# Kernel optimization log

Hardware: AMD Instinct MI355X
Metric: run time of the kernel (lower is better)

Reference implementation:

```python
import jax, jax.numpy as jnp
import numpy as np

LATENT = 256


def setup_inputs() -> dict:
    key = jax.random.key(0)
    ks = jax.random.split(key, 10)
    B, T, V, E, D0, H, L = 512, 200, 3356, 1128, 20000, 1024, LATENT

    def glorot(k, shape):
        fan_out, fan_in = shape
        std = np.sqrt(2.0 / (fan_in + fan_out)).astype(np.float32)
        return jax.random.normal(k, shape, dtype=jnp.float32) * std

    x = jax.random.uniform(ks[0], (B, D0), dtype=jnp.float32)
    item_ids = jax.random.randint(ks[1], (B, T), 0, V, dtype=jnp.int32)
    embed = jax.random.normal(ks[2], (V, E), dtype=jnp.float32)
    Wi = glorot(ks[3], (L, E))
    bi = jnp.zeros((L,), jnp.float32)
    We1 = glorot(ks[4], (H, D0))
    be1 = jnp.zeros((H,), jnp.float32)
    We2 = glorot(ks[5], (2 * L, H))
    be2 = jnp.zeros((2 * L,), jnp.float32)
    Wd1 = glorot(ks[6], (H, L))
    bd1 = jnp.zeros((H,), jnp.float32)
    Wd2 = glorot(ks[7], (D0, H))
    bd2 = jnp.zeros((D0,), jnp.float32)
    # dropout(p=0.5) mask, pre-scaled by 1/(1-p)=2
    drop_mask = (jax.random.bernoulli(ks[8], 0.5, (B, D0))).astype(jnp.float32) * 2.0
    eps = jax.random.normal(ks[9], (B, L), dtype=jnp.float32)
    return {"x": x, "item_ids": item_ids, "embed": embed, "Wi": Wi, "bi": bi,
            "We1": We1, "be1": be1, "We2": We2, "be2": be2,
            "Wd1": Wd1, "bd1": bd1, "Wd2": Wd2, "bd2": bd2,
            "drop_mask": drop_mask, "eps": eps}


def reference(x, item_ids, embed, Wi, bi, We1, be1, We2, be2,
              Wd1, bd1, Wd2, bd2, drop_mask, eps):
    # item feature path: embedding lookup -> linear -> per-sequence stats
    item = jnp.einsum('bte,le->btl', embed[item_ids], Wi) + bi        # [B,T,L]
    mean = jnp.mean(item, axis=1)                                      # [B,L]
    deviation = jnp.std(item, axis=1, ddof=1)                          # torch.std (unbiased)

    # encoder: F.normalize (L2 over features) -> dropout -> tanh MLP
    xn = x / jnp.maximum(jnp.linalg.norm(x, axis=1, keepdims=True), 1e-12)
    h = xn * drop_mask
    h = jnp.tanh(h @ We1.T + be1)
    gparams = h @ We2.T + be2                                          # [B,2L]
    mu, logvar = gparams[:, :LATENT], gparams[:, LATENT:]

    # reparam: MVN with diagonal covariance diag(deviation) == mean + sqrt(dev)*eps
    prior = mean + jnp.sqrt(deviation) * eps
    z = prior * jnp.exp(0.5 * logvar) + mu

    # decoder: tanh MLP
    hd = jnp.tanh(z @ Wd1.T + bd1)
    recon_x = hd @ Wd2.T + bd2                                         # [B,D0]
    return recon_x, mu, logvar
```

## Files before the change

kernel.cpp:

```cpp
#include <hip/hip_runtime.h>
#include <hip/hip_bf16.h>

typedef __bf16 bf16x8 __attribute__((ext_vector_type(8)));
typedef float f32x4 __attribute__((ext_vector_type(4)));
typedef unsigned short u16x8 __attribute__((ext_vector_type(8)));
typedef unsigned int u32x4 __attribute__((ext_vector_type(4)));

static __device__ __forceinline__ unsigned short f2bf(float f){
  unsigned int u = __float_as_uint(f);
  u += 0x7fffu + ((u >> 16) & 1u);
  return (unsigned short)(u >> 16);
}

static __device__ __forceinline__ unsigned int cvtpk(float lo, float hi){
  unsigned int r;
  asm("v_cvt_pk_bf16_f32 %0, %1, %2" : "=v"(r) : "v"(lo), "v"(hi));
  return r;
}

static __device__ __forceinline__ u16x8 cvt8(const float4& a, const float4& b){
  u16x8 r;
  r[0]=f2bf(a.x); r[1]=f2bf(a.y); r[2]=f2bf(a.z); r[3]=f2bf(a.w);
  r[4]=f2bf(b.x); r[5]=f2bf(b.y); r[6]=f2bf(b.z); r[7]=f2bf(b.w);
  return r;
}

static __device__ __forceinline__ void gload16(const void* g, void* l){
  __builtin_amdgcn_global_load_lds(
      (const __attribute__((address_space(1))) unsigned int*)g,
      (__attribute__((address_space(3))) unsigned int*)l, 16, 0, 0);
}

template<int EPI>
__global__ __launch_bounds__(256, 2) void gemm_bigf(
    const unsigned short* __restrict__ A, const float* __restrict__ Bw,
    const float* __restrict__ bias,
    float* __restrict__ Cf, unsigned short* __restrict__ Cbf,
    int M, int N, int K, int kchunk)
{
  constexpr int BK = 32, BUFB = 8192 + 16384;
  __shared__ char smem[3 * BUFB];

  const int tid  = threadIdx.x, lane = tid & 63, wave = tid >> 6;
  const int bm0  = blockIdx.y * 128, bn0 = blockIdx.x * 128;
  const int k0   = blockIdx.z * kchunk;
  const int kend = min(K, k0 + kchunk);
  const int nk   = (kend - k0) / BK;
  const int fr = lane & 15, fq = lane >> 4;
  const int wm = (wave >> 1) * 64, wn = (wave & 1) * 64;

  const int ar_off = wave * 16 + (lane >> 2), ac_off = (lane & 3) * 8;
  const int br_off = wave * 8 + (lane >> 3);
  const int bg_off = (((lane & 7) ^ (lane >> 3)) << 2);

  auto stage = [&](int buf, int t){
    char* base = smem + buf * BUFB;
    const int kk = k0 + t * BK;
    #pragma unroll
    for (int c = 0; c < 2; c++) {
      const int r = min(bm0 + c * 64 + ar_off, M - 1);
      gload16(A + (size_t)r * K + kk + ac_off, base + c * 4096 + wave * 1024);
    }
    #pragma unroll
    for (int c = 0; c < 4; c++) {
      const int r = min(bn0 + c * 32 + br_off, N - 1);
      gload16(Bw + (size_t)r * K + kk + bg_off, base + 8192 + c * 4096 + wave * 1024);
    }
  };

  stage(0, 0);
  if (nk > 1) stage(1, 1);
  if (nk > 2) stage(2, 2);

  f32x4 acc[4][4] = {};
  int cur = 0;

  for (int t = 0; t < nk; ++t) {
    const int rem = nk - t - 1;
    if (rem >= 2)      asm volatile("s_waitcnt vmcnt(12)" ::: "memory");
    else if (rem == 1) asm volatile("s_waitcnt vmcnt(6)"  ::: "memory");
    else               asm volatile("s_waitcnt vmcnt(0)"  ::: "memory");
    __builtin_amdgcn_s_barrier();
    __builtin_amdgcn_sched_barrier(0);

    const unsigned short* lA = (const unsigned short*)(smem + cur * BUFB);
    const char*           lB = smem + cur * BUFB + 8192;
    u16x8 af[4], bg[4];
    #pragma unroll
    for (int i = 0; i < 4; i++) af[i] = *(const u16x8*)&lA[(wm + i*16 + fr) * BK + fq * 8];
    #pragma unroll
    for (int j = 0; j < 4; j++) {
      const int r  = wn + j*16 + fr;
      const int s0 = (((fq << 1) ^ (r & 7)) << 4);
      const char* bp = lB + r * 128;
      f32x4 u = *(const f32x4*)(bp + s0);
      f32x4 v = *(const f32x4*)(bp + (s0 ^ 16));
      u32x4 wv; wv[0]=cvtpk(u[0],u[1]); wv[1]=cvtpk(u[2],u[3]);
                wv[2]=cvtpk(v[0],v[1]); wv[3]=cvtpk(v[2],v[3]);
      bg[j] = __builtin_bit_cast(u16x8, wv);
    }
    asm volatile("s_waitcnt lgkmcnt(0)" ::: "memory");
    __builtin_amdgcn_sched_barrier(0);
    __builtin_amdgcn_s_barrier();
    if (t + 3 < nk) stage(cur, t + 3);

    #pragma unroll
    for (int i = 0; i < 4; i++)
      #pragma unroll
      for (int j = 0; j < 4; j++)
        acc[i][j] = __builtin_amdgcn_mfma_f32_16x16x32_bf16(
            __builtin_bit_cast(bf16x8, af[i]),
            __builtin_bit_cast(bf16x8, bg[j]),
            acc[i][j], 0, 0, 0);
    cur = (cur == 2) ? 0 : cur + 1;
  }

  #pragma unroll
  for (int i = 0; i < 4; i++)
    #pragma unroll
    for (int j = 0; j < 4; j++)
      #pragma unroll
      for (int r = 0; r < 4; r++) {
        int row = bm0 + wm + i*16 + fq*4 + r;
        int col = bn0 + wn + j*16 + fr;
        if (row < M && col < N) {
          float v = acc[i][j][r];
          if constexpr (EPI == 0) {
            Cf[(size_t)row * N + col] = v + (bias ? bias[col] : 0.0f);
          } else if constexpr (EPI == 1) {
            atomicAdd(&Cf[(size_t)row * N + col], v);
          } else {
            Cbf[(size_t)row * N + col] = f2bf(tanhf(v + bias[col]));
          }
        }
      }
}

template<int EPI>
__global__ __launch_bounds__(256) void gemm_sm(
    const unsigned short* __restrict__ A, const unsigned short* __restrict__ Bw,
    const float* __restrict__ bias,
    float* __restrict__ Cf, unsigned short* __restrict__ Cbf,
    int M, int N, int K, int kchunk)
{
  constexpr int BM = 128, BN = 128, BK = 32;
  __shared__ unsigned short lds[(BM + BN) * BK];
  unsigned short* lA = lds;
  unsigned short* lB = lds + BM * BK;

  const int tid  = threadIdx.x, lane = tid & 63, wave = tid >> 6;
  const int bm0  = blockIdx.y * BM, bn0 = blockIdx.x * BN;
  const int k0   = blockIdx.z * kchunk;
  const int kend = min(K, k0 + kchunk);
  const int fr = lane & 15, fq = lane >> 4;
  const int wm = (wave >> 1) * 64, wn = (wave & 1) * 64;

  const bool isA  = wave < 2;
  const int cbase = (wave & 1) * 4;
  const int srow  = lane >> 2, scol = (lane & 3) * 8;
  const unsigned short* G = isA ? A : Bw;
  const int glim = (isA ? M : N) - 1;
  const int g0   = isA ? bm0 : bn0;
  unsigned short* ldst = isA ? lA : lB;

  f32x4 acc[4][4] = {};

  for (int kk = k0; kk < kend; kk += BK) {
    #pragma unroll
    for (int c = 0; c < 4; c++) {
      const int ch = cbase + c;
      const int r = min(g0 + ch * 16 + srow, glim);
      gload16(G + (size_t)r * K + kk + scol, (char*)ldst + ch * 1024);
    }
    __syncthreads();
    u16x8 af[4], bg[4];
    #pragma unroll
    for (int i = 0; i < 4; i++) af[i] = *(const u16x8*)&lA[(wm + i*16 + fr) * BK + fq * 8];
    #pragma unroll
    for (int j = 0; j < 4; j++) bg[j] = *(const u16x8*)&lB[(wn + j*16 + fr) * BK + fq * 8];
    #pragma unroll
    for (int i = 0; i < 4; i++)
      #pragma unroll
      for (int j = 0; j < 4; j++)
        acc[i][j] = __builtin_amdgcn_mfma_f32_16x16x32_bf16(
            __builtin_bit_cast(bf16x8, af[i]),
            __builtin_bit_cast(bf16x8, bg[j]),
            acc[i][j], 0, 0, 0);
    __syncthreads();
  }

  #pragma unroll
  for (int i = 0; i < 4; i++)
    #pragma unroll
    for (int j = 0; j < 4; j++)
      #pragma unroll
      for (int r = 0; r < 4; r++) {
        int row = bm0 + wm + i*16 + fq*4 + r;
        int col = bn0 + wn + j*16 + fr;
        if (row < M && col < N) {
          float v = acc[i][j][r];
          if constexpr (EPI == 0) {
            Cf[(size_t)row * N + col] = v + (bias ? bias[col] : 0.0f);
          } else if constexpr (EPI == 1) {
            atomicAdd(&Cf[(size_t)row * N + col], v);
          } else {
            Cbf[(size_t)row * N + col] = f2bf(tanhf(v + bias[col]));
          }
        }
      }
}

__global__ __launch_bounds__(256) void cvt4_kernel(
    const float* __restrict__ s0, unsigned short* __restrict__ d0, int n0,
    const float* __restrict__ s1, unsigned short* __restrict__ d1, int n1,
    const float* __restrict__ s2, unsigned short* __restrict__ d2, int n2,
    const float* __restrict__ s3, unsigned short* __restrict__ d3, int n3)
{
  int i = (blockIdx.x * 256 + threadIdx.x) * 8;
  const float* s; unsigned short* d;
  if (i < n0)            { s = s0; d = d0; }
  else if ((i -= n0) < n1) { s = s1; d = d1; }
  else if ((i -= n1) < n2) { s = s2; d = d2; }
  else if ((i -= n2) < n3) { s = s3; d = d3; }
  else return;
  const float4* q = (const float4*)(s + i);
  *(u16x8*)(d + i) = cvt8(q[0], q[1]);
}

__global__ __launch_bounds__(256) void cvtpad_kernel(
    const float* __restrict__ src, unsigned short* __restrict__ dst,
    int rows, int scols, int dcols)
{
  int i8 = blockIdx.x * 256 + threadIdx.x;
  int c8 = dcols / 8;
  if (i8 >= rows * c8) return;
  int r = i8 / c8, c0 = (i8 % c8) * 8;
  const float* s = src + (size_t)r * scols;
  u16x8 o;
  #pragma unroll
  for (int e = 0; e < 8; e++) { int c = c0 + e; o[e] = (c < scols) ? f2bf(s[c]) : (unsigned short)0; }
  *(u16x8*)(dst + (size_t)r * dcols + c0) = o;
}

__global__ __launch_bounds__(256) void ynorm_kernel(
    const float* __restrict__ x, const float* __restrict__ dm,
    unsigned short* __restrict__ y, float* __restrict__ ninv, int D0)
{
  const int b = blockIdx.x, tid = threadIdx.x;
  const float4* x4 = (const float4*)(x + (size_t)b * D0);
  const float4* d4 = (const float4*)(dm + (size_t)b * D0);
  ushort4* y4 = (ushort4*)(y + (size_t)b * D0);
  const int n4 = D0 / 4;
  float ss = 0.f;
  for (int i = tid; i < n4; i += 256) {
    float4 xv = x4[i], dv = d4[i];
    ss += xv.x*xv.x + xv.y*xv.y + xv.z*xv.z + xv.w*xv.w;
    ushort4 o;
    o.x = f2bf(xv.x*dv.x); o.y = f2bf(xv.y*dv.y);
    o.z = f2bf(xv.z*dv.z); o.w = f2bf(xv.w*dv.w);
    y4[i] = o;
  }
  #pragma unroll
  for (int off = 32; off > 0; off >>= 1) ss += __shfl_down(ss, off);
  __shared__ float wsum[4];
  if ((tid & 63) == 0) wsum[tid >> 6] = ss;
  __syncthreads();
  if (tid == 0) {
    float t = wsum[0] + wsum[1] + wsum[2] + wsum[3];
    ninv[b] = 1.0f / fmaxf(sqrtf(t), 1e-12f);
  }
}

__global__ __launch_bounds__(256) void stats_kernel(
    const float* __restrict__ proj, const int* __restrict__ ids,
    const float* __restrict__ bi, const float* __restrict__ eps,
    float* __restrict__ prior, int T)
{
  const int b = blockIdx.x, l = threadIdx.x;
  __shared__ int sid[256];
  if (l < T) sid[l] = ids[b * T + l];
  __syncthreads();
  float s1 = 0.f, s2 = 0.f;
  #pragma unroll 4
  for (int t = 0; t < T; t++) {
    float p = proj[(size_t)sid[t] * 256 + l];
    s1 += p; s2 += p * p;
  }
  float var = fmaxf((s2 - s1 * s1 / (float)T) / (float)(T - 1), 0.f);
  float dev = sqrtf(var);
  float mean = s1 / (float)T + bi[l];
  prior[b * 256 + l] = mean + sqrtf(dev) * eps[b * 256 + l];
}

__global__ __launch_bounds__(256) void epi1_kernel(
    const float* __restrict__ C1, const float* __restrict__ ninv,
    const float* __restrict__ be1, unsigned short* __restrict__ h)
{
  int i = blockIdx.x * 256 + threadIdx.x;
  int b = i >> 10, n = i & 1023;
  h[i] = f2bf(tanhf(ninv[b] * C1[i] + be1[n]));
}

__global__ __launch_bounds__(256) void z_kernel(
    const float* __restrict__ gp, const float* __restrict__ prior,
    const float* __restrict__ be2,
    float* __restrict__ out_mu, float* __restrict__ out_lv,
    unsigned short* __restrict__ z)
{
  int i = blockIdx.x * 256 + threadIdx.x;
  int b = i >> 8, l = i & 255;
  float mu = gp[b * 512 + l]       + be2[l];
  float lv = gp[b * 512 + 256 + l] + be2[256 + l];
  out_mu[i] = mu;
  out_lv[i] = lv;
  z[i] = f2bf(prior[i] * expf(0.5f * lv) + mu);
}

extern "C" void kernel_launch(void* const* d_in, const int* in_sizes, int n_in,
                              void* d_out, int out_size, void* d_ws, size_t ws_size,
                              hipStream_t stream)
{
  const float* x     = (const float*)d_in[0];
  const int*   ids   = (const int*)  d_in[1];
  const float* embed = (const float*)d_in[2];
  const float* Wi    = (const float*)d_in[3];
  const float* bi    = (const float*)d_in[4];
  const float* We1   = (const float*)d_in[5];
  const float* be1   = (const float*)d_in[6];
  const float* We2   = (const float*)d_in[7];
  const float* be2   = (const float*)d_in[8];
  const float* Wd1   = (const float*)d_in[9];
  const float* bd1   = (const float*)d_in[10];
  const float* Wd2   = (const float*)d_in[11];
  const float* bd2   = (const float*)d_in[12];
  const float* dm    = (const float*)d_in[13];
  const float* eps   = (const float*)d_in[14];

  constexpr int B = 512, T = 200, V = 3356, E = 1128, Ep = 1152, D0 = 20000, H = 1024, L = 256;

  char* w = (char*)d_ws;
  auto carve = [&](size_t bytes) { char* p = w; w += (bytes + 255) & ~(size_t)255; return p; };
  unsigned short* We2b  = (unsigned short*)carve((size_t)2 * L * H * 2);
  unsigned short* Wd1b  = (unsigned short*)carve((size_t)H * L * 2);
  unsigned short* embedb= (unsigned short*)carve((size_t)V * Ep * 2);
  unsigned short* Wib   = (unsigned short*)carve((size_t)L * Ep * 2);
  float*          proj  = (float*)         carve((size_t)V * L * 4);
  unsigned short* y     = (unsigned short*)carve((size_t)B * D0 * 2);
  float*          C1    = (float*)         carve((size_t)B * H * 4);
  unsigned short* h     = (unsigned short*)carve((size_t)B * H * 2);
  float*          gp    = (float*)         carve((size_t)B * 2 * L * 4);
  float*          prior = (float*)         carve((size_t)B * L * 4);
  unsigned short* z     = (unsigned short*)carve((size_t)B * L * 2);
  unsigned short* hd    = (unsigned short*)carve((size_t)B * H * 2);
  float*          ninv  = (float*)         carve((size_t)B * 4);

  float* out_recon = (float*)d_out;
  float* out_mu    = out_recon + (size_t)B * D0;
  float* out_lv    = out_mu + (size_t)B * L;

  {
    const int n0 = 2 * L * H, n1 = H * L;
    cvt4_kernel<<<(n0 + n1) / (8 * 256), 256, 0, stream>>>(
        We2, We2b, n0, Wd1, Wd1b, n1, We2, We2b, 0, We2, We2b, 0);
  }
  cvtpad_kernel<<<(V * (Ep/8) + 255) / 256, 256, 0, stream>>>(embed, embedb, V, E, Ep);
  cvtpad_kernel<<<(L * (Ep/8) + 255) / 256, 256, 0, stream>>>(Wi, Wib, L, E, Ep);

  ynorm_kernel<<<B, 256, 0, stream>>>(x, dm, y, ninv, D0);

  hipMemsetAsync(proj, 0, (size_t)V * L * 4, stream);
  gemm_sm<1><<<dim3(2, 27, 4), 256, 0, stream>>>(
      embedb, Wib, nullptr, proj, nullptr, V, L, Ep, 288);
  stats_kernel<<<B, 256, 0, stream>>>(proj, ids, bi, eps, prior, T);

  hipMemsetAsync(C1, 0, (size_t)B * H * 4, stream);
  gemm_bigf<1><<<dim3(8, 4, 25), 256, 0, stream>>>(
      y, We1, nullptr, C1, nullptr, B, H, D0, 800);
  epi1_kernel<<<(B * H) / 256, 256, 0, stream>>>(C1, ninv, be1, h);

  hipMemsetAsync(gp, 0, (size_t)B * 2 * L * 4, stream);
  gemm_sm<1><<<dim3(4, 4, 4), 256, 0, stream>>>(
      h, We2b, nullptr, gp, nullptr, B, 2 * L, H, 256);
  z_kernel<<<(B * L) / 256, 256, 0, stream>>>(gp, prior, be2, out_mu, out_lv, z);

  gemm_sm<2><<<dim3(8, 4, 1), 256, 0, stream>>>(
      z, Wd1b, bd1, nullptr, hd, B, H, L, 256);
  gemm_bigf<0><<<dim3(157, 4, 1), 256, 0, stream>>>(
      hd, Wd2, bd2, out_recon, nullptr, B, D0, H, 1024);
}
```

Before: 287.3 us.

## Pipeline small bf16 GEMMs with triple buffering, add XCD-aware block remap

Rewrites the small bf16 GEMM kernel to use a three-stage LDS ring. Async global-to-LDS loads for later K tiles are issued while MFMA runs on the current tile, using explicit vmcnt waits and barriers in place of the old load-sync-compute-sync loop. Both GEMM kernels now remap workgroup IDs so that blocks sharing tiles land on the same XCD, aiming for better L2 locality. The weight-convert kernel becomes grid-stride with 16 elements per thread. This raises LDS use in the small GEMM and depends on the hand-set waitcnt values being correct.

```diff
diff --git a/kernel.cpp b/kernel.cpp
--- a/kernel.cpp
+++ b/kernel.cpp
@@ -29,6 +29,13 @@
   __builtin_amdgcn_global_load_lds(
       (const __attribute__((address_space(1))) unsigned int*)g,
       (__attribute__((address_space(3))) unsigned int*)l, 16, 0, 0);
+}
+
+static __device__ __forceinline__ int xcd_remap(int o, int nwg){
+  const int NX = 8;
+  int q = nwg / NX, r = nwg % NX;
+  int xcd = o % NX, pos = o / NX;
+  return (xcd < r ? xcd * (q + 1) : r * (q + 1) + (xcd - r) * q) + pos;
 }
 
 template<int EPI>
@@ -41,9 +48,16 @@
   constexpr int BK = 32, BUFB = 8192 + 16384;
   __shared__ char smem[3 * BUFB];
 
+  const int gx = gridDim.x, gy = gridDim.y;
+  const int nwg = gx * gy * gridDim.z;
+  int o = blockIdx.x + gx * (blockIdx.y + gy * blockIdx.z);
+  int vv = xcd_remap(o, nwg);
+  const int bxi = vv % gx; vv /= gx;
+  const int byi = vv % gy; const int bzi = vv / gy;
+
   const int tid  = threadIdx.x, lane = tid & 63, wave = tid >> 6;
-  const int bm0  = blockIdx.y * 128, bn0 = blockIdx.x * 128;
-  const int k0   = blockIdx.z * kchunk;
+  const int bm0  = byi * 128, bn0 = bxi * 128;
+  const int k0   = bzi * kchunk;
   const int kend = min(K, k0 + kchunk);
   const int nk   = (kend - k0) / BK;
   const int fr = lane & 15, fq = lane >> 4;
@@ -124,33 +138,38 @@
         int row = bm0 + wm + i*16 + fq*4 + r;
         int col = bn0 + wn + j*16 + fr;
         if (row < M && col < N) {
-          float v = acc[i][j][r];
+          float v2 = acc[i][j][r];
           if constexpr (EPI == 0) {
-            Cf[(size_t)row * N + col] = v + (bias ? bias[col] : 0.0f);
+            Cf[(size_t)row * N + col] = v2 + (bias ? bias[col] : 0.0f);
           } else if constexpr (EPI == 1) {
-            atomicAdd(&Cf[(size_t)row * N + col], v);
+            atomicAdd(&Cf[(size_t)row * N + col], v2);
           } else {
-            Cbf[(size_t)row * N + col] = f2bf(tanhf(v + bias[col]));
+            Cbf[(size_t)row * N + col] = f2bf(tanhf(v2 + bias[col]));
           }
         }
       }
 }
 
 template<int EPI>
-__global__ __launch_bounds__(256) void gemm_sm(
+__global__ __launch_bounds__(256) void gemm_bf(
     const unsigned short* __restrict__ A, const unsigned short* __restrict__ Bw,
     const float* __restrict__ bias,
     float* __restrict__ Cf, unsigned short* __restrict__ Cbf,
     int M, int N, int K, int kchunk)
 {
-  constexpr int BM = 128, BN = 128, BK = 32;
-  __shared__ unsigned short lds[(BM + BN) * BK];
-  unsigned short* lA = lds;
-  unsigned short* lB = lds + BM * BK;
+  constexpr int BM = 128, BN = 128, BK = 32, BUF = (BM + BN) * BK;
+  __shared__ unsigned short lds[3 * BUF];
+
+  const int gx = gridDim.x, gy = gridDim.y;
+  const int nwg = gx * gy * gridDim.z;
+  int o = blockIdx.x + gx * (blockIdx.y + gy * blockIdx.z);
+  int v = xcd_remap(o, nwg);
+  const int bx = v % gx; v /= gx;
+  const int by = v % gy; const int bz = v / gy;
 
   const int tid  = threadIdx.x, lane = tid & 63, wave = tid >> 6;
-  const int bm0  = blockIdx.y * BM, bn0 = blockIdx.x * BN;
-  const int k0   = blockIdx.z * kchunk;
+  const int bm0  = by * BM, bn0 = bx * BN;
+  const int k0   = bz * kchunk;
   const int kend = min(K, k0 + kchunk);
   const int fr = lane & 15, fq = lane >> 4;
   const int wm = (wave >> 1) * 64, wn = (wave & 1) * 64;
@@ -161,23 +180,44 @@
   const unsigned short* G = isA ? A : Bw;
   const int glim = (isA ? M : N) - 1;
   const int g0   = isA ? bm0 : bn0;
-  unsigned short* ldst = isA ? lA : lB;
-
-  f32x4 acc[4][4] = {};
-
-  for (int kk = k0; kk < kend; kk += BK) {
+  const int loff = isA ? 0 : BM * BK;
+
+  const int nk = (kend - k0) / BK;
+
+  auto stage = [&](int buf, int t){
+    unsigned short* dst = lds + buf * BUF + loff;
+    const int kk = k0 + t * BK;
     #pragma unroll
     for (int c = 0; c < 4; c++) {
       const int ch = cbase + c;
       const int r = min(g0 + ch * 16 + srow, glim);
-      gload16(G + (size_t)r * K + kk + scol, (char*)ldst + ch * 1024);
+      gload16(G + (size_t)r * K + kk + scol, (char*)dst + ch * 1024);
     }
-    __syncthreads();
+  };
+
+  if (nk > 0) stage(0, 0);
+  if (nk > 1) stage(1, 1);
+  if (nk > 2) stage(2, 2);
+
+  f32x4 acc[4][4] = {};
+  int cur = 0;
+
+  for (int t = 0; t < nk; ++t) {
+    const int rem = nk - t - 1;
+    if (rem >= 2)      asm volatile("s_waitcnt vmcnt(8)" ::: "memory");
+    else if (rem == 1) asm volatile("s_waitcnt vmcnt(4)" ::: "memory");
+    else               asm volatile("s_waitcnt vmcnt(0)" ::: "memory");
+    __builtin_amdgcn_s_barrier();
+    __builtin_amdgcn_sched_barrier(0);
+
+    const unsigned short* lA = lds + cur * BUF;
+    const unsigned short* lB = lA + BM * BK;
     u16x8 af[4], bg[4];
     #pragma unroll
     for (int i = 0; i < 4; i++) af[i] = *(const u16x8*)&lA[(wm + i*16 + fr) * BK + fq * 8];
     #pragma unroll
     for (int j = 0; j < 4; j++) bg[j] = *(const u16x8*)&lB[(wn + j*16 + fr) * BK + fq * 8];
+
     #pragma unroll
     for (int i = 0; i < 4; i++)
       #pragma unroll
@@ -186,7 +226,12 @@
             __builtin_bit_cast(bf16x8, af[i]),
             __builtin_bit_cast(bf16x8, bg[j]),
             acc[i][j], 0, 0, 0);
-    __syncthreads();
+
+    asm volatile("s_waitcnt lgkmcnt(0)" ::: "memory");
+    __builtin_amdgcn_sched_barrier(0);
+    __builtin_amdgcn_s_barrier();
+    if (t + 3 < nk) stage(cur, t + 3);
+    cur = (cur == 2) ? 0 : cur + 1;
   }
 
   #pragma unroll
@@ -198,13 +243,13 @@
         int row = bm0 + wm + i*16 + fq*4 + r;
         int col = bn0 + wn + j*16 + fr;
         if (row < M && col < N) {
-          float v = acc[i][j][r];
+          float v2 = acc[i][j][r];
           if constexpr (EPI == 0) {
-            Cf[(size_t)row * N + col] = v + (bias ? bias[col] : 0.0f);
+            Cf[(size_t)row * N + col] = v2 + (bias ? bias[col] : 0.0f);
           } else if constexpr (EPI == 1) {
-            atomicAdd(&Cf[(size_t)row * N + col], v);
+            atomicAdd(&Cf[(size_t)row * N + col], v2);
           } else {
-            Cbf[(size_t)row * N + col] = f2bf(tanhf(v + bias[col]));
+            Cbf[(size_t)row * N + col] = f2bf(tanhf(v2 + bias[col]));
           }
         }
       }
@@ -214,17 +259,22 @@
     const float* __restrict__ s0, unsigned short* __restrict__ d0, int n0,
     const float* __restrict__ s1, unsigned short* __restrict__ d1, int n1,
     const float* __restrict__ s2, unsigned short* __restrict__ d2, int n2,
-    const float* __restrict__ s3, unsigned short* __restrict__ d3, int n3)
-{
-  int i = (blockIdx.x * 256 + threadIdx.x) * 8;
-  const float* s; unsigned short* d;
-  if (i < n0)            { s = s0; d = d0; }
-  else if ((i -= n0) < n1) { s = s1; d = d1; }
-  else if ((i -= n1) < n2) { s = s2; d = d2; }
-  else if ((i -= n2) < n3) { s = s3; d = d3; }
-  else return;
-  const float4* q = (const float4*)(s + i);
-  *(u16x8*)(d + i) = cvt8(q[0], q[1]);
+    const float* __restrict__ s3, unsigned short* __restrict__ d3, int n3,
+    int nunits16)
+{
+  const int stride = gridDim.x * 256;
+  for (int u = blockIdx.x * 256 + threadIdx.x; u < nunits16; u += stride) {
+    int i = u * 16;
+    const float* s; unsigned short* d;
+    if (i < n0)              { s = s0; d = d0; }
+    else if ((i -= n0) < n1) { s = s1; d = d1; }
+    else if ((i -= n1) < n2) { s = s2; d = d2; }
+    else                     { i -= n2; s = s3; d = d3; }
+    const float4* q = (const float4*)(s + i);
+    float4 a0 = q[0], a1 = q[1], a2 = q[2], a3 = q[3];
+    *(u16x8*)(d + i)     = cvt8(a0, a1);
+    *(u16x8*)(d + i + 8) = cvt8(a2, a3);
+  }
 }
 
 __global__ __launch_bounds__(256) void cvtpad_kernel(
@@ -360,8 +410,9 @@
 
   {
     const int n0 = 2 * L * H, n1 = H * L;
-    cvt4_kernel<<<(n0 + n1) / (8 * 256), 256, 0, stream>>>(
-        We2, We2b, n0, Wd1, Wd1b, n1, We2, We2b, 0, We2, We2b, 0);
+    const int nunits16 = (n0 + n1) / 16;
+    cvt4_kernel<<<192, 256, 0, stream>>>(We2, We2b, n0, Wd1, Wd1b, n1,
+                                         We2, We2b, 0, We2, We2b, 0, nunits16);
   }
   cvtpad_kernel<<<(V * (Ep/8) + 255) / 256, 256, 0, stream>>>(embed, embedb, V, E, Ep);
   cvtpad_kernel<<<(L * (Ep/8) + 255) / 256, 256, 0, stream>>>(Wi, Wib, L, E, Ep);
@@ -369,7 +420,7 @@
   ynorm_kernel<<<B, 256, 0, stream>>>(x, dm, y, ninv, D0);
 
   hipMemsetAsync(proj, 0, (size_t)V * L * 4, stream);
-  gemm_sm<1><<<dim3(2, 27, 4), 256, 0, stream>>>(
+  gemm_bf<1><<<dim3(2, 27, 4), 256, 0, stream>>>(
       embedb, Wib, nullptr, proj, nullptr, V, L, Ep, 288);
   stats_kernel<<<B, 256, 0, stream>>>(proj, ids, bi, eps, prior, T);
 
@@ -379,11 +430,11 @@
   epi1_kernel<<<(B * H) / 256, 256, 0, stream>>>(C1, ninv, be1, h);
 
   hipMemsetAsync(gp, 0, (size_t)B * 2 * L * 4, stream);
-  gemm_sm<1><<<dim3(4, 4, 4), 256, 0, stream>>>(
+  gemm_bf<1><<<dim3(4, 4, 4), 256, 0, stream>>>(
       h, We2b, nullptr, gp, nullptr, B, 2 * L, H, 256);
   z_kernel<<<(B * L) / 256, 256, 0, stream>>>(gp, prior, be2, out_mu, out_lv, z);
 
-  gemm_sm<2><<<dim3(8, 4, 1), 256, 0, stream>>>(
+  gemm_bf<2><<<dim3(8, 4, 1), 256, 0, stream>>>(
       z, Wd1b, bd1, nullptr, hd, B, H, L, 256);
   gemm_bigf<0><<<dim3(157, 4, 1), 256, 0, stream>>>(
       hd, Wd2, bd2, out_recon, nullptr, B, D0, H, 1024);
```

Measured after the change: 273.8 us. -4.7%, faster.
